# Kernel optimization log

Hardware: AMD Instinct MI355X
Metric: run time of the kernel (lower is better)

## Reference

```python
import jax, jax.numpy as jnp
import numpy as np

RES_SCALE = 0.1
B, C, H, W = 16, 256, 96, 96


def conv3x3(x, w):
    # NCHW input, OIHW weight, SAME padding (padding=1 for k=3), no bias
    return jax.lax.conv_general_dilated(
        x, w, window_strides=(1, 1), padding="SAME",
        dimension_numbers=("NCHW", "OIHW", "NCHW"))


def setup_inputs() -> dict:
    key = jax.random.key(0)
    k1, k2, k3, k4 = jax.random.split(key, 4)
    fan = C * 9
    x = jax.random.normal(k1, (B, C, H, W), dtype=jnp.float32)
    conv2_w = jax.random.normal(k2, (C, C, 3, 3), dtype=jnp.float32) / np.sqrt(fan)
    conv3_w = jax.random.normal(k3, (C, C, 3, 3), dtype=jnp.float32) / np.sqrt(fan)
    prelu_w = jnp.full((1,), 0.25, dtype=jnp.float32)  # nn.PReLU default init
    # interleaved channel partition: P=0::3 (86), R=1::3 (85), T=2::3 (85)
    idx_p = jnp.arange(0, C, 3, dtype=jnp.int32)
    idx_r = jnp.arange(1, C, 3, dtype=jnp.int32)
    idx_t = jnp.arange(2, C, 3, dtype=jnp.int32)
    return {"x": x, "conv2_w": conv2_w, "conv3_w": conv3_w, "prelu_w": prelu_w,
            "idx_p": idx_p, "idx_r": idx_r, "idx_t": idx_t}


def reference(x, conv2_w, conv3_w, prelu_w, idx_p, idx_r, idx_t):
    # op2 = conv2(prune(x, skip_gate)) ; all-ones gate -> identity prune
    op2 = conv3x3(x, conv2_w)  # [B, C, H, W]
    # per-channel activation routing (gathers permute channel order to [P,R,T])
    gp = op2[:, idx_p]                                  # [B, 86, H, W]
    a = jnp.concatenate([
        jnp.where(gp >= 0, gp, prelu_w[0] * gp),        # PReLU (1 shared param)
        jax.nn.relu(op2[:, idx_r]),                     # [B, 85, H, W]
        jnp.tanh(op2[:, idx_t]),                        # [B, 85, H, W]
    ], axis=1)                                          # [B, C, H, W]
    # conv_tot branch: op3 = conv3(a)*res_scale + x * reshape(skip_conv_gate)
    # skip_conv_gate == ones here, so the skip scaling is identity
    op3 = conv3x3(a, conv3_w) * RES_SCALE + x
    return op3


if __name__ == "__main__":
    out = reference(**setup_inputs())
    print(out.shape, out.dtype)
```

## Files before the change

kernel.cpp:

```cpp
#include <hip/hip_runtime.h>
#include <math.h>


#define Bn 16
#define Cn 256
#define Hn 96
#define Wn 96
#define PH 98
#define PW 98
#define HW (Hn*Wn)

typedef __bf16 bf16x8 __attribute__((ext_vector_type(8)));
typedef float  f32x4  __attribute__((ext_vector_type(4)));

__device__ __forceinline__ unsigned short f2bf(float f) {
    unsigned int u = __float_as_uint(f);
    unsigned int r = (u + 0x7fffu + ((u >> 16) & 1u)) >> 16;
    return (unsigned short)r;
}

__device__ __forceinline__ void lds_load16(void* lds, const void* g) {
    auto gp = (const __attribute__((address_space(1))) char*)(unsigned long long)(uintptr_t)g;
    auto lp = (__attribute__((address_space(3))) char*)(unsigned int)(uintptr_t)lds;
    __builtin_amdgcn_global_load_lds(gp, lp, 16, 0, 0);
}

#define SB() __builtin_amdgcn_sched_barrier(0)
#define MEMFENCE() asm volatile("" ::: "memory")

__global__ __launch_bounds__(256)
void zero_border_k(unsigned short* __restrict__ t) {
    int idx = blockIdx.x * 256 + threadIdx.x;
    int oct = idx & 31;
    int rest = idx >> 5;
    int pidx = rest % 388;
    int b = rest / 388;
    int h, w;
    if (pidx < 98)       { h = 0;  w = pidx; }
    else if (pidx < 196) { h = 97; w = pidx - 98; }
    else if (pidx < 292) { h = pidx - 196 + 1; w = 0; }
    else                 { h = pidx - 292 + 1; w = 97; }
    size_t e = ((size_t)(b * PH + h) * PW + w) * 256 + oct * 8;
    *(uint4*)(t + e) = make_uint4(0u, 0u, 0u, 0u);
}

template<bool PERM>
__global__ __launch_bounds__(256)
void pack_w_k(const float* __restrict__ w, unsigned short* __restrict__ wp) {
    int idx = blockIdx.x * 256 + threadIdx.x;
    int ci_l = idx & 31;
    int c    = (idx >> 5) & 255;
    int v    = idx >> 13;
    int k9   = v % 9;
    int cc   = v / 9;
    int co;
    if (PERM) {
        co = (c < 86) ? c * 3 : (c < 171) ? (c - 86) * 3 + 1 : (c - 171) * 3 + 2;
    } else {
        co = c;
    }
    float val = w[((size_t)co * 256 + cc * 32 + ci_l) * 9 + k9];
    wp[idx] = f2bf(val);
}

__global__ __launch_bounds__(256)
void transform_x_k(const float* __restrict__ x, unsigned short* __restrict__ xp) {
    __shared__ float s[32 * 33];
    const int t = threadIdx.x;
    const int col0 = blockIdx.x * 32;
    const int row  = blockIdx.y;
    const int z = blockIdx.z;
    const int b = z >> 3;
    const int ci0 = (z & 7) * 32;

    #pragma unroll
    for (int i = 0; i < 4; ++i) {
        int ci = i * 8 + (t >> 5);
        int px = t & 31;
        s[ci * 33 + px] = x[((size_t)(b * Cn + ci0 + ci)) * HW + row * Wn + col0 + px];
    }
    __syncthreads();
    const int px = t >> 3;
    const int c4 = (t & 7) * 4;
    ushort4 o;
    o.x = f2bf(s[(c4 + 0) * 33 + px]);
    o.y = f2bf(s[(c4 + 1) * 33 + px]);
    o.z = f2bf(s[(c4 + 2) * 33 + px]);
    o.w = f2bf(s[(c4 + 3) * 33 + px]);
    size_t e = ((size_t)(b * PH + row + 1) * PW + (col0 + px + 1)) * 256 + ci0 + c4;
    *(ushort4*)(xp + e) = o;
}

template<int MODE>
__global__ __launch_bounds__(256, 2)
void conv_k(const unsigned short* __restrict__ in_cl,
            const unsigned short* __restrict__ wp,
            const float* __restrict__ prelu_w,
            const float* __restrict__ xres,
            void* __restrict__ outp)
{
    __shared__ unsigned short s_x[2][2048 * 8];

    const int tid = threadIdx.x;
    const int bid = blockIdx.x;
    const int wg = (bid & 7) * 192 + (bid >> 3);
    const int co_base = (wg & 3) * 64;
    const int t2 = wg >> 2;
    const int tile = t2 % 24;
    const int b = t2 / 24;
    const int R0 = (tile / 3) * 12;
    const int C0 = (tile % 3) * 32;

    const int lane = tid & 63;
    const int wv = tid >> 6;
    const int l15 = lane & 15;
    const int qq = lane >> 4;

    const unsigned short* img = in_cl + (size_t)b * PH * PW * 256;

    int xg[8];
    #pragma unroll
    for (int i = 0; i < 8; ++i) {
        int slot = i * 256 + tid;
        int lsl = slot ^ ((slot >> 3) & 3);
        if (lsl > 1903) lsl = 1903;
        int p = lsl >> 2;
        int pr = p / 34, pc = p - pr * 34;
        xg[i] = ((R0 + pr) * PW + (C0 + pc)) * 256 + (lsl & 3) * 8;
    }
    int aoff[4];
    #pragma unroll
    for (int m = 0; m < 4; ++m)
        aoff[m] = (co_base + m * 16 + l15) * 32 + qq * 8;

    f32x4 acc[4][6];
    #pragma unroll
    for (int m = 0; m < 4; ++m)
        #pragma unroll
        for (int n = 0; n < 6; ++n) acc[m][n] = 0.f;

    bf16x8 A0[4], A1[4];

    #pragma unroll
    for (int i = 0; i < 8; ++i)
        lds_load16(&s_x[0][(size_t)(i * 256 + tid) * 8], img + xg[i]);
    #pragma unroll
    for (int m = 0; m < 4; ++m)
        A0[m] = *(const bf16x8*)(wp + aoff[m]);
    MEMFENCE(); SB();
    asm volatile("s_waitcnt vmcnt(0)" ::: "memory");
    SB();
    __builtin_amdgcn_s_barrier();
    SB();

#define REGION(K9, AUSE, ALD) {                                                   \
                               \
    _Pragma("unroll")                                                             \
    for (int m = 0; m < 4; ++m)                                                   \
        ALD[m] = *(const bf16x8*)(wpc + (K9 + 1) * 8192 + aoff[m]);               \
    MEMFENCE(); SB();                                                             \
                                           \
    if ((K9) < 8)                                                                 \
        lds_load16(&sxn[(size_t)((K9) * 256 + tid) * 8], img + xg[(K9)] + cn32);  \
    MEMFENCE(); SB();                                                             \
                                                            \
    bf16x8 bf[6];                                                                 \
    {                                                                             \
        const int kh_ = (K9) / 3, kw_ = (K9) - 3 * ((K9) / 3);                    \
        _Pragma("unroll")                                                         \
        for (int n = 0; n < 6; ++n) {                                             \
            const int P_ = (wv * 3 + (n >> 1) + kh_) * 34 + (n & 1) * 16 + l15 + kw_; \
            bf[n] = *(const bf16x8*)&sxc[P_ * 32 + ((qq ^ ((P_ >> 1) & 3)) << 3)]; \
        }                                                                         \
    }                                                                             \
    asm volatile("s_waitcnt lgkmcnt(0)" ::: "memory");                            \
    SB();                                                                         \
    __builtin_amdgcn_s_setprio(1);                                                \
    _Pragma("unroll")                                                             \
    for (int n = 0; n < 6; ++n)                                                   \
        _Pragma("unroll")                                                         \
        for (int m = 0; m < 4; ++m)                                               \
            acc[m][n] = __builtin_amdgcn_mfma_f32_16x16x32_bf16(AUSE[m], bf[n], acc[m][n], 0, 0, 0); \
    __builtin_amdgcn_s_setprio(0);                                                \
    SB();                                                                         \
    if ((K9) < 8) { asm volatile("s_waitcnt vmcnt(1)" ::: "memory"); }            \
    else          { asm volatile("s_waitcnt vmcnt(0)" ::: "memory"); }            \
    SB();                                                                         \
    if ((K9) == 8) { __builtin_amdgcn_s_barrier(); SB(); }                        \
}

#define CHUNK_EVEN() { \
    REGION(0, A0, A1) REGION(1, A1, A0) REGION(2, A0, A1)                         \
    REGION(3, A1, A0) REGION(4, A0, A1) REGION(5, A1, A0)                         \
    REGION(6, A0, A1) REGION(7, A1, A0) REGION(8, A0, A1) }
#define CHUNK_ODD() { \
    REGION(0, A1, A0) REGION(1, A0, A1) REGION(2, A1, A0)                         \
    REGION(3, A0, A1) REGION(4, A1, A0) REGION(5, A0, A1)                         \
    REGION(6, A1, A0) REGION(7, A0, A1) REGION(8, A1, A0) }

    for (int c2 = 0; c2 < 4; ++c2) {
        {
            const int c = 2 * c2;
            const unsigned short* wpc = wp + (size_t)c * 73728;
            const unsigned short* sxc = s_x[0];
            unsigned short* sxn = s_x[1];
            const int cn32 = ((c + 1) & 7) * 32;
            CHUNK_EVEN()
        }
        {
            const int c = 2 * c2 + 1;
            const unsigned short* wpc = wp + (size_t)c * 73728;
            const unsigned short* sxc = s_x[1];
            unsigned short* sxn = s_x[0];
            const int cn32 = ((c + 1) & 7) * 32;
            CHUNK_ODD()
        }
    }
#undef REGION
#undef CHUNK_EVEN
#undef CHUNK_ODD

    if constexpr (MODE == 0) {
        const float pw = prelu_w[0];
        unsigned short* aout = (unsigned short*)outp;
        #pragma unroll
        for (int n = 0; n < 6; ++n) {
            const int row_p = wv * 3 + (n >> 1);
            const int col_p = (n & 1) * 16 + l15;
            size_t pix = ((size_t)(b * PH + R0 + row_p + 1)) * PW + (C0 + col_p + 1);
            #pragma unroll
            for (int m = 0; m < 4; ++m) {
                const int cb = co_base + m * 16 + qq * 4;
                float r[4];
                #pragma unroll
                for (int j = 0; j < 4; ++j) {
                    const int ch = cb + j;
                    float s = acc[m][n][j];
                    if (ch < 86)        r[j] = s >= 0.f ? s : pw * s;
                    else if (ch < 171)  r[j] = fmaxf(s, 0.f);
                    else {
                        float e = __expf(2.f * s);
                        r[j] = 1.f - 2.f / (e + 1.f);
                    }
                }
                ushort4 o;
                o.x = f2bf(r[0]); o.y = f2bf(r[1]); o.z = f2bf(r[2]); o.w = f2bf(r[3]);
                *(ushort4*)(aout + pix * 256 + cb) = o;
            }
        }
    } else {
        float* fout = (float*)outp;
        #pragma unroll
        for (int n = 0; n < 6; ++n) {
            const int row_p = wv * 3 + (n >> 1);
            const int col_p = (n & 1) * 16 + l15;
            #pragma unroll
            for (int m = 0; m < 4; ++m) {
                const int cb = co_base + m * 16 + qq * 4;
                size_t base = ((size_t)(b * Cn + cb)) * HW + (size_t)(R0 + row_p) * Wn + (C0 + col_p);
                #pragma unroll
                for (int j = 0; j < 4; ++j)
                    fout[base + (size_t)j * HW] = acc[m][n][j] * 0.1f + xres[base + (size_t)j * HW];
            }
        }
    }
}

extern "C" void kernel_launch(void* const* d_in, const int* in_sizes, int n_in,
                              void* d_out, int out_size, void* d_ws, size_t ws_size,
                              hipStream_t stream) {
    const float* x  = (const float*)d_in[0];
    const float* w2 = (const float*)d_in[1];
    const float* w3 = (const float*)d_in[2];
    const float* pw = (const float*)d_in[3];
    float* out = (float*)d_out;
    char* ws = (char*)d_ws;

    unsigned short* a_cl = (unsigned short*)ws;
    unsigned short* wp2  = (unsigned short*)(ws + 78675968);
    unsigned short* wp3  = (unsigned short*)(ws + 78675968 + 1179648);
    unsigned short* x_pad = (unsigned short*)d_out;

    zero_border_k<<<776, 256, 0, stream>>>(x_pad);
    zero_border_k<<<776, 256, 0, stream>>>(a_cl);
    pack_w_k<true ><<<2304, 256, 0, stream>>>(w2, wp2);
    pack_w_k<false><<<2304, 256, 0, stream>>>(w3, wp3);
    transform_x_k<<<dim3(3, 96, 128), 256, 0, stream>>>(x, x_pad);

    conv_k<0><<<1536, 256, 0, stream>>>(x_pad, wp2, pw, nullptr, (void*)a_cl);
    conv_k<1><<<1536, 256, 0, stream>>>(a_cl, wp3, nullptr, x, (void*)out);
}
```

Measured before the change: 412.2 us.

## Triple-buffer weight registers and relax waitcnt to deepen global-load prefetch

Weight fragments now rotate through three register buffers, so they are prefetched two taps ahead instead of one. The per-tap lgkmcnt(0) wait and vmcnt(1/0) waits are replaced by specific vmcnt thresholds, which keeps more global loads in flight while MFMAs run. The chunk loop is collapsed into one loop over c that alternates the LDS buffer, and the next-chunk LDS load is skipped on the last chunk. This adds register pressure, and the hand-counted vmcnt values must match the actual number of outstanding loads. Dropping the explicit lgkmcnt wait relies on the compiler to insert LDS waits itself. The loads at tap 7 and 8 also read weights past the current chunk, and on the last chunk past the end of the weight array.

New measurement: 757.2 us. +83.7%, slower.

```diff
diff --git a/kernel.cpp b/kernel.cpp
--- a/kernel.cpp
+++ b/kernel.cpp
@@ -139,86 +139,74 @@
         #pragma unroll
         for (int n = 0; n < 6; ++n) acc[m][n] = 0.f;
 
-    bf16x8 A0[4], A1[4];
+    bf16x8 A[3][4];
 
     #pragma unroll
     for (int i = 0; i < 8; ++i)
         lds_load16(&s_x[0][(size_t)(i * 256 + tid) * 8], img + xg[i]);
     #pragma unroll
-    for (int m = 0; m < 4; ++m)
-        A0[m] = *(const bf16x8*)(wp + aoff[m]);
+    for (int m = 0; m < 4; ++m) A[0][m] = *(const bf16x8*)(wp + aoff[m]);
+    #pragma unroll
+    for (int m = 0; m < 4; ++m) A[1][m] = *(const bf16x8*)(wp + 8192 + aoff[m]);
     MEMFENCE(); SB();
     asm volatile("s_waitcnt vmcnt(0)" ::: "memory");
     SB();
     __builtin_amdgcn_s_barrier();
     SB();
 
-#define REGION(K9, AUSE, ALD) {                                                   \
-                               \
+#define REGION(K9, VN) {                                                          \
+    constexpr int AU_ = (K9) % 3;                                                 \
+    constexpr int AL_ = ((K9) + 2) % 3;                                           \
     _Pragma("unroll")                                                             \
     for (int m = 0; m < 4; ++m)                                                   \
-        ALD[m] = *(const bf16x8*)(wpc + (K9 + 1) * 8192 + aoff[m]);               \
+        A[AL_][m] = *(const bf16x8*)(wpc + ((K9) + 2) * 8192 + aoff[m]);          \
     MEMFENCE(); SB();                                                             \
-                                           \
-    if ((K9) < 8)                                                                 \
-        lds_load16(&sxn[(size_t)((K9) * 256 + tid) * 8], img + xg[(K9)] + cn32);  \
+    if ((K9) < 8 && c < 7)                                                        \
+        lds_load16(&sxn[(size_t)((K9) * 256 + tid) * 8],                          \
+                   img + xg[(K9)] + (c + 1) * 32);                                \
     MEMFENCE(); SB();                                                             \
-                                                            \
     bf16x8 bf[6];                                                                 \
     {                                                                             \
-        const int kh_ = (K9) / 3, kw_ = (K9) - 3 * ((K9) / 3);                    \
+        constexpr int kh_ = (K9) / 3, kw_ = (K9) - 3 * ((K9) / 3);                \
         _Pragma("unroll")                                                         \
         for (int n = 0; n < 6; ++n) {                                             \
             const int P_ = (wv * 3 + (n >> 1) + kh_) * 34 + (n & 1) * 16 + l15 + kw_; \
             bf[n] = *(const bf16x8*)&sxc[P_ * 32 + ((qq ^ ((P_ >> 1) & 3)) << 3)]; \
         }                                                                         \
     }                                                                             \
-    asm volatile("s_waitcnt lgkmcnt(0)" ::: "memory");                            \
-    SB();                                                                         \
+    if ((VN) == 10) { asm volatile("s_waitcnt vmcnt(10)" ::: "memory"); SB(); }   \
+    if ((VN) == 11) { asm volatile("s_waitcnt vmcnt(11)" ::: "memory"); SB(); }   \
     __builtin_amdgcn_s_setprio(1);                                                \
     _Pragma("unroll")                                                             \
     for (int n = 0; n < 6; ++n)                                                   \
         _Pragma("unroll")                                                         \
         for (int m = 0; m < 4; ++m)                                               \
-            acc[m][n] = __builtin_amdgcn_mfma_f32_16x16x32_bf16(AUSE[m], bf[n], acc[m][n], 0, 0, 0); \
+            acc[m][n] = __builtin_amdgcn_mfma_f32_16x16x32_bf16(A[AU_][m], bf[n], acc[m][n], 0, 0, 0); \
     __builtin_amdgcn_s_setprio(0);                                                \
     SB();                                                                         \
-    if ((K9) < 8) { asm volatile("s_waitcnt vmcnt(1)" ::: "memory"); }            \
-    else          { asm volatile("s_waitcnt vmcnt(0)" ::: "memory"); }            \
-    SB();                                                                         \
-    if ((K9) == 8) { __builtin_amdgcn_s_barrier(); SB(); }                        \
-}
-
-#define CHUNK_EVEN() { \
-    REGION(0, A0, A1) REGION(1, A1, A0) REGION(2, A0, A1)                         \
-    REGION(3, A1, A0) REGION(4, A0, A1) REGION(5, A1, A0)                         \
-    REGION(6, A0, A1) REGION(7, A1, A0) REGION(8, A0, A1) }
-#define CHUNK_ODD() { \
-    REGION(0, A1, A0) REGION(1, A0, A1) REGION(2, A1, A0)                         \
-    REGION(3, A0, A1) REGION(4, A1, A0) REGION(5, A0, A1)                         \
-    REGION(6, A1, A0) REGION(7, A0, A1) REGION(8, A1, A0) }
-
-    for (int c2 = 0; c2 < 4; ++c2) {
-        {
-            const int c = 2 * c2;
-            const unsigned short* wpc = wp + (size_t)c * 73728;
-            const unsigned short* sxc = s_x[0];
-            unsigned short* sxn = s_x[1];
-            const int cn32 = ((c + 1) & 7) * 32;
-            CHUNK_EVEN()
-        }
-        {
-            const int c = 2 * c2 + 1;
-            const unsigned short* wpc = wp + (size_t)c * 73728;
-            const unsigned short* sxc = s_x[1];
-            unsigned short* sxn = s_x[0];
-            const int cn32 = ((c + 1) & 7) * 32;
-            CHUNK_ODD()
-        }
+}
+
+    for (int c = 0; c < 8; ++c) {
+        const unsigned short* wpc = wp + (size_t)c * 73728;
+        const unsigned short* sxc = s_x[c & 1];
+        unsigned short* sxn = s_x[(c + 1) & 1];
+
+        REGION(0, -1)
+        REGION(1, 10)
+        REGION(2, 11)
+        REGION(3, 11)
+        REGION(4, 11)
+        REGION(5, 11)
+        REGION(6, 11)
+        REGION(7, 11)
+        REGION(8, 10)
+
+        asm volatile("s_waitcnt vmcnt(4)" ::: "memory");
+        SB();
+        __builtin_amdgcn_s_barrier();
+        SB();
     }
 #undef REGION
-#undef CHUNK_EVEN
-#undef CHUNK_ODD
 
     if constexpr (MODE == 0) {
         const float pw = prelu_w[0];
```
